# Kernel tuning notes

Measured on AMD Instinct MI355X. Metric: run time of the kernel, lower is better.

Reference implementation:

```python
import jax, jax.numpy as jnp
import numpy as np

A = 5.0  # smoothness parameter 'a'

def setup_inputs() -> dict:
    key = jax.random.key(0)
    kx, kw = jax.random.split(key)
    x = jax.random.uniform(kx, (1024, 512), dtype=jnp.float32)
    weight = jax.random.uniform(kw, (512, 512), dtype=jnp.float32)
    return {"x": x, "weight": weight}

def reference(x, weight):
    # inner: [batch, in, out] broadcast min
    inner = jnp.minimum(x[..., None], weight[None])
    # smooth union (smooth max) over the 'in' dim: logsumexp(a*z)/a
    smooth = jax.scipy.special.logsumexp(A * inner, axis=-2) / A
    hard = jnp.max(inner, axis=-2)
    # straight-through: forward value = hard, gradient flows through smooth
    return jax.lax.stop_gradient(hard - smooth) + smooth
```

## Files before the change

kernel.cpp:

```cpp
#include <hip/hip_runtime.h>


#define MDIM 1024
#define KDIM 512
#define NDIM 512
#define MB 8
#define NT 256
#define KW 64
#define NWAVE 8

__device__ __forceinline__ float bcast(float v, int srcLane) {
    return __int_as_float(__builtin_amdgcn_readlane(__float_as_int(v), srcLane));
}

__global__ __launch_bounds__(512, 2) void tropical_r9(
    const float* __restrict__ x,
    const float* __restrict__ w,
    float* __restrict__ out)
{
    const int tid  = threadIdx.x;
    const int lane = tid & 63;
    const int wv   = tid >> 6;
    const int m0   = blockIdx.x * MB;
    const int n0   = blockIdx.y * NT;
    const int k0   = wv * KW;

    __shared__ float red[NWAVE][MB][NT];

    float xreg[MB];
#pragma unroll
    for (int r = 0; r < MB; ++r)
        xreg[r] = x[(size_t)(m0 + r) * KDIM + k0 + lane];

    const float4* __restrict__ wb =
        (const float4*)(w + (size_t)k0 * NDIM + n0) + lane;

    float acc[MB][4];
#pragma unroll
    for (int r = 0; r < MB; ++r)
#pragma unroll
        for (int j = 0; j < 4; ++j) acc[r][j] = 0.0f;

    float4 cA = wb[0 * 128], cB = wb[1 * 128];
    float4 cC = wb[2 * 128], cD = wb[3 * 128];

#pragma unroll 2
    for (int kc = 0; kc < KW; kc += 4) {
        float4 nA, nB, nC, nD;
        if (kc + 4 < KW) {
            nA = wb[(size_t)(kc + 4) * 128]; nB = wb[(size_t)(kc + 5) * 128];
            nC = wb[(size_t)(kc + 6) * 128]; nD = wb[(size_t)(kc + 7) * 128];
        }
        float xb0[MB], xb1[MB], xb2[MB], xb3[MB];
#pragma unroll
        for (int r = 0; r < MB; ++r) {
            xb0[r] = bcast(xreg[r], kc);
            xb1[r] = bcast(xreg[r], kc + 1);
            xb2[r] = bcast(xreg[r], kc + 2);
            xb3[r] = bcast(xreg[r], kc + 3);
        }
#pragma unroll
        for (int r = 0; r < MB; ++r) {
            acc[r][0] = fmaxf(acc[r][0], fmaxf(fminf(xb0[r], cA.x), fminf(xb1[r], cB.x)));
            acc[r][1] = fmaxf(acc[r][1], fmaxf(fminf(xb0[r], cA.y), fminf(xb1[r], cB.y)));
            acc[r][2] = fmaxf(acc[r][2], fmaxf(fminf(xb0[r], cA.z), fminf(xb1[r], cB.z)));
            acc[r][3] = fmaxf(acc[r][3], fmaxf(fminf(xb0[r], cA.w), fminf(xb1[r], cB.w)));
            acc[r][0] = fmaxf(acc[r][0], fmaxf(fminf(xb2[r], cC.x), fminf(xb3[r], cD.x)));
            acc[r][1] = fmaxf(acc[r][1], fmaxf(fminf(xb2[r], cC.y), fminf(xb3[r], cD.y)));
            acc[r][2] = fmaxf(acc[r][2], fmaxf(fminf(xb2[r], cC.z), fminf(xb3[r], cD.z)));
            acc[r][3] = fmaxf(acc[r][3], fmaxf(fminf(xb2[r], cC.w), fminf(xb3[r], cD.w)));
        }
        cA = nA; cB = nB; cC = nC; cD = nD;
    }

#pragma unroll
    for (int r = 0; r < MB; ++r) {
        float4 v; v.x = acc[r][0]; v.y = acc[r][1]; v.z = acc[r][2]; v.w = acc[r][3];
        ((float4*)&red[wv][r][0])[lane] = v;
    }
    __syncthreads();

    {
        const int r  = tid >> 6;
        const int c4 = tid & 63;
        float4 v = ((const float4*)&red[0][r][0])[c4];
#pragma unroll
        for (int q = 1; q < NWAVE; ++q) {
            float4 u = ((const float4*)&red[q][r][0])[c4];
            v.x = fmaxf(v.x, u.x); v.y = fmaxf(v.y, u.y);
            v.z = fmaxf(v.z, u.z); v.w = fmaxf(v.w, u.w);
        }
        *(float4*)(out + (size_t)(m0 + r) * NDIM + n0 + 4 * c4) = v;
    }
}

extern "C" void kernel_launch(void* const* d_in, const int* in_sizes, int n_in,
                              void* d_out, int out_size, void* d_ws, size_t ws_size,
                              hipStream_t stream) {
    const float* x = (const float*)d_in[0];
    const float* w = (const float*)d_in[1];
    float* out = (float*)d_out;

    dim3 grid(MDIM / MB, NDIM / NT);
    tropical_r9<<<grid, dim3(512), 0, stream>>>(x, w, out);
}
```

Baseline: 77.08 us.

## Stagger per-block K windows and deepen weight prefetch to two stages

Each wave's k-window is rotated by block indices, and its starting row within the window is offset by block, so concurrent blocks read different weight rows. This aims to reduce channel or cache contention. Weight loads are also prefetched two steps ahead instead of one. The extra register buffer may raise register pressure, and the wrapped index math adds a few redundant loads at the end.

```diff
diff --git a/kernel.cpp b/kernel.cpp
--- a/kernel.cpp
+++ b/kernel.cpp
@@ -13,7 +13,7 @@
     return __int_as_float(__builtin_amdgcn_readlane(__float_as_int(v), srcLane));
 }
 
-__global__ __launch_bounds__(512, 2) void tropical_r9(
+__global__ __launch_bounds__(512, 2) void tropical_r11(
     const float* __restrict__ x,
     const float* __restrict__ w,
     float* __restrict__ out)
@@ -21,9 +21,14 @@
     const int tid  = threadIdx.x;
     const int lane = tid & 63;
     const int wv   = tid >> 6;
-    const int m0   = blockIdx.x * MB;
-    const int n0   = blockIdx.y * NT;
-    const int k0   = wv * KW;
+    const int bm   = blockIdx.x;
+    const int bn   = blockIdx.y;
+    const int m0   = bm * MB;
+    const int n0   = bn * NT;
+
+    const int win = (wv + bm + (bn << 2)) & 7;
+    const int k0  = win * KW;
+    const int r0  = (bm & 15) * 4;
 
     __shared__ float red[NWAVE][MB][NT];
 
@@ -41,36 +46,41 @@
 #pragma unroll
         for (int j = 0; j < 4; ++j) acc[r][j] = 0.0f;
 
-    float4 cA = wb[0 * 128], cB = wb[1 * 128];
-    float4 cC = wb[2 * 128], cD = wb[3 * 128];
+    float4 A0 = wb[(size_t)(r0 + 0) * 128], A1 = wb[(size_t)(r0 + 1) * 128];
+    float4 A2 = wb[(size_t)(r0 + 2) * 128], A3 = wb[(size_t)(r0 + 3) * 128];
+    int kp = (r0 + 4) & 63;
+    float4 B0 = wb[(size_t)(kp + 0) * 128], B1 = wb[(size_t)(kp + 1) * 128];
+    float4 B2 = wb[(size_t)(kp + 2) * 128], B3 = wb[(size_t)(kp + 3) * 128];
 
+    int kr = r0;
 #pragma unroll 2
-    for (int kc = 0; kc < KW; kc += 4) {
-        float4 nA, nB, nC, nD;
-        if (kc + 4 < KW) {
-            nA = wb[(size_t)(kc + 4) * 128]; nB = wb[(size_t)(kc + 5) * 128];
-            nC = wb[(size_t)(kc + 6) * 128]; nD = wb[(size_t)(kc + 7) * 128];
-        }
+    for (int i = 0; i < 16; ++i) {
+        const int kn = (kr + 8) & 63;
+        float4 C0 = wb[(size_t)(kn + 0) * 128], C1 = wb[(size_t)(kn + 1) * 128];
+        float4 C2 = wb[(size_t)(kn + 2) * 128], C3 = wb[(size_t)(kn + 3) * 128];
+
         float xb0[MB], xb1[MB], xb2[MB], xb3[MB];
 #pragma unroll
         for (int r = 0; r < MB; ++r) {
-            xb0[r] = bcast(xreg[r], kc);
-            xb1[r] = bcast(xreg[r], kc + 1);
-            xb2[r] = bcast(xreg[r], kc + 2);
-            xb3[r] = bcast(xreg[r], kc + 3);
+            xb0[r] = bcast(xreg[r], kr);
+            xb1[r] = bcast(xreg[r], kr + 1);
+            xb2[r] = bcast(xreg[r], kr + 2);
+            xb3[r] = bcast(xreg[r], kr + 3);
         }
 #pragma unroll
         for (int r = 0; r < MB; ++r) {
-            acc[r][0] = fmaxf(acc[r][0], fmaxf(fminf(xb0[r], cA.x), fminf(xb1[r], cB.x)));
-            acc[r][1] = fmaxf(acc[r][1], fmaxf(fminf(xb0[r], cA.y), fminf(xb1[r], cB.y)));
-            acc[r][2] = fmaxf(acc[r][2], fmaxf(fminf(xb0[r], cA.z), fminf(xb1[r], cB.z)));
-            acc[r][3] = fmaxf(acc[r][3], fmaxf(fminf(xb0[r], cA.w), fminf(xb1[r], cB.w)));
-            acc[r][0] = fmaxf(acc[r][0], fmaxf(fminf(xb2[r], cC.x), fminf(xb3[r], cD.x)));
-            acc[r][1] = fmaxf(acc[r][1], fmaxf(fminf(xb2[r], cC.y), fminf(xb3[r], cD.y)));
-            acc[r][2] = fmaxf(acc[r][2], fmaxf(fminf(xb2[r], cC.z), fminf(xb3[r], cD.z)));
-            acc[r][3] = fmaxf(acc[r][3], fmaxf(fminf(xb2[r], cC.w), fminf(xb3[r], cD.w)));
+            acc[r][0] = fmaxf(acc[r][0], fmaxf(fminf(xb0[r], A0.x), fminf(xb1[r], A1.x)));
+            acc[r][1] = fmaxf(acc[r][1], fmaxf(fminf(xb0[r], A0.y), fminf(xb1[r], A1.y)));
+            acc[r][2] = fmaxf(acc[r][2], fmaxf(fminf(xb0[r], A0.z), fminf(xb1[r], A1.z)));
+            acc[r][3] = fmaxf(acc[r][3], fmaxf(fminf(xb0[r], A0.w), fminf(xb1[r], A1.w)));
+            acc[r][0] = fmaxf(acc[r][0], fmaxf(fminf(xb2[r], A2.x), fminf(xb3[r], A3.x)));
+            acc[r][1] = fmaxf(acc[r][1], fmaxf(fminf(xb2[r], A2.y), fminf(xb3[r], A3.y)));
+            acc[r][2] = fmaxf(acc[r][2], fmaxf(fminf(xb2[r], A2.z), fminf(xb3[r], A3.z)));
+            acc[r][3] = fmaxf(acc[r][3], fmaxf(fminf(xb2[r], A2.w), fminf(xb3[r], A3.w)));
         }
-        cA = nA; cB = nB; cC = nC; cD = nD;
+        A0 = B0; A1 = B1; A2 = B2; A3 = B3;
+        B0 = C0; B1 = C1; B2 = C2; B3 = C3;
+        kr = (kr + 4) & 63;
     }
 
 #pragma unroll
@@ -102,5 +112,5 @@
     float* out = (float*)d_out;
 
     dim3 grid(MDIM / MB, NDIM / NT);
-    tropical_r9<<<grid, dim3(512), 0, stream>>>(x, w, out);
+    tropical_r11<<<grid, dim3(512), 0, stream>>>(x, w, out);
 }
```

Measured after the change: 76.91 us. Within noise of the previous version (-0.2%).

## Pack inputs to fp16 pairs and use packed half min/max accumulation

Applied to the files above, without the earlier changes.

Adds a pre-pass kernel that converts x and the weight matrix to fp16, packing pairs of k values into 32-bit words. The main kernel then does the min/max reduction with packed half2 operations, handling two k values per instruction, and reads x through scalar loads instead of lane broadcasts. The goal is to halve the VALU instruction count and the weight bandwidth. In exchange it adds a second launch, and the result is computed in fp16, so the output is rounded to half precision rather than exact fp32.

```diff
diff --git a/kernel.cpp b/kernel.cpp
--- a/kernel.cpp
+++ b/kernel.cpp
@@ -1,21 +1,47 @@
 #include <hip/hip_runtime.h>
 
+
+typedef _Float16 h2 __attribute__((ext_vector_type(2)));
+typedef unsigned int uint32;
 
 #define MDIM 1024
 #define KDIM 512
 #define NDIM 512
-#define MB 8
-#define NT 256
-#define KW 64
+#define K2   (KDIM / 2)
+#define MB   8
+#define NT   256
 #define NWAVE 8
+#define KP   (K2 / NWAVE)
 
-__device__ __forceinline__ float bcast(float v, int srcLane) {
-    return __int_as_float(__builtin_amdgcn_readlane(__float_as_int(v), srcLane));
+__device__ __forceinline__ h2 h2min(h2 a, h2 b) { return __builtin_elementwise_min(a, b); }
+__device__ __forceinline__ h2 h2max(h2 a, h2 b) { return __builtin_elementwise_max(a, b); }
+
+__global__ __launch_bounds__(512) void pack_f16(const float* __restrict__ x,
+                                                const float* __restrict__ w,
+                                                uint32* __restrict__ xp,
+                                                uint32* __restrict__ wp)
+{
+    const int b = blockIdx.x, tid = threadIdx.x;
+    if (b < 256) {
+        const int idx = b * 512 + tid;
+        const int k2 = idx >> 9, n = idx & 511;
+        h2 v;
+        v[0] = (_Float16)w[(size_t)(2 * k2) * NDIM + n];
+        v[1] = (_Float16)w[(size_t)(2 * k2 + 1) * NDIM + n];
+        wp[idx] = __builtin_bit_cast(uint32, v);
+    } else {
+        const int idx = (b - 256) * 512 + tid;
+        const float2 f = ((const float2*)x)[idx];
+        h2 v;
+        v[0] = (_Float16)f.x;
+        v[1] = (_Float16)f.y;
+        xp[idx] = __builtin_bit_cast(uint32, v);
+    }
 }
 
-__global__ __launch_bounds__(512, 2) void tropical_r9(
-    const float* __restrict__ x,
-    const float* __restrict__ w,
+__global__ __launch_bounds__(512, 2) void tropical_h16(
+    const uint32* __restrict__ xp,
+    const uint32* __restrict__ wp,
     float* __restrict__ out)
 {
     const int tid  = threadIdx.x;
@@ -23,59 +49,44 @@
     const int wv   = tid >> 6;
     const int m0   = blockIdx.x * MB;
     const int n0   = blockIdx.y * NT;
-    const int k0   = wv * KW;
+    const int kp0  = __builtin_amdgcn_readfirstlane(wv * KP);
 
     __shared__ float red[NWAVE][MB][NT];
 
-    float xreg[MB];
-#pragma unroll
-    for (int r = 0; r < MB; ++r)
-        xreg[r] = x[(size_t)(m0 + r) * KDIM + k0 + lane];
+    const uint4* __restrict__ wb =
+        (const uint4*)(wp + (size_t)kp0 * NDIM + n0) + lane;
+    const uint32* __restrict__ xr0 = xp + (size_t)m0 * K2 + kp0;
 
-    const float4* __restrict__ wb =
-        (const float4*)(w + (size_t)k0 * NDIM + n0) + lane;
-
-    float acc[MB][4];
+    h2 acc[MB][4];
 #pragma unroll
     for (int r = 0; r < MB; ++r)
 #pragma unroll
-        for (int j = 0; j < 4; ++j) acc[r][j] = 0.0f;
+        for (int j = 0; j < 4; ++j) acc[r][j] = (h2)0;
 
-    float4 cA = wb[0 * 128], cB = wb[1 * 128];
-    float4 cC = wb[2 * 128], cD = wb[3 * 128];
+    uint4 A = wb[0], B = wb[(size_t)128];
 
 #pragma unroll 2
-    for (int kc = 0; kc < KW; kc += 4) {
-        float4 nA, nB, nC, nD;
-        if (kc + 4 < KW) {
-            nA = wb[(size_t)(kc + 4) * 128]; nB = wb[(size_t)(kc + 5) * 128];
-            nC = wb[(size_t)(kc + 6) * 128]; nD = wb[(size_t)(kc + 7) * 128];
-        }
-        float xb0[MB], xb1[MB], xb2[MB], xb3[MB];
+    for (int i = 0; i < KP; ++i) {
+        uint4 C;
+        if (i + 2 < KP) C = wb[(size_t)(i + 2) * 128];
 #pragma unroll
         for (int r = 0; r < MB; ++r) {
-            xb0[r] = bcast(xreg[r], kc);
-            xb1[r] = bcast(xreg[r], kc + 1);
-            xb2[r] = bcast(xreg[r], kc + 2);
-            xb3[r] = bcast(xreg[r], kc + 3);
+            const h2 xv = __builtin_bit_cast(h2, xr0[(size_t)r * K2 + i]);
+            acc[r][0] = h2max(acc[r][0], h2min(xv, __builtin_bit_cast(h2, A.x)));
+            acc[r][1] = h2max(acc[r][1], h2min(xv, __builtin_bit_cast(h2, A.y)));
+            acc[r][2] = h2max(acc[r][2], h2min(xv, __builtin_bit_cast(h2, A.z)));
+            acc[r][3] = h2max(acc[r][3], h2min(xv, __builtin_bit_cast(h2, A.w)));
         }
-#pragma unroll
-        for (int r = 0; r < MB; ++r) {
-            acc[r][0] = fmaxf(acc[r][0], fmaxf(fminf(xb0[r], cA.x), fminf(xb1[r], cB.x)));
-            acc[r][1] = fmaxf(acc[r][1], fmaxf(fminf(xb0[r], cA.y), fminf(xb1[r], cB.y)));
-            acc[r][2] = fmaxf(acc[r][2], fmaxf(fminf(xb0[r], cA.z), fminf(xb1[r], cB.z)));
-            acc[r][3] = fmaxf(acc[r][3], fmaxf(fminf(xb0[r], cA.w), fminf(xb1[r], cB.w)));
-            acc[r][0] = fmaxf(acc[r][0], fmaxf(fminf(xb2[r], cC.x), fminf(xb3[r], cD.x)));
-            acc[r][1] = fmaxf(acc[r][1], fmaxf(fminf(xb2[r], cC.y), fminf(xb3[r], cD.y)));
-            acc[r][2] = fmaxf(acc[r][2], fmaxf(fminf(xb2[r], cC.z), fminf(xb3[r], cD.z)));
-            acc[r][3] = fmaxf(acc[r][3], fmaxf(fminf(xb2[r], cC.w), fminf(xb3[r], cD.w)));
-        }
-        cA = nA; cB = nB; cC = nC; cD = nD;
+        A = B; B = C;
     }
 
 #pragma unroll
     for (int r = 0; r < MB; ++r) {
-        float4 v; v.x = acc[r][0]; v.y = acc[r][1]; v.z = acc[r][2]; v.w = acc[r][3];
+        float4 v;
+        v.x = fmaxf((float)acc[r][0][0], (float)acc[r][0][1]);
+        v.y = fmaxf((float)acc[r][1][0], (float)acc[r][1][1]);
+        v.z = fmaxf((float)acc[r][2][0], (float)acc[r][2][1]);
+        v.w = fmaxf((float)acc[r][3][0], (float)acc[r][3][1]);
         ((float4*)&red[wv][r][0])[lane] = v;
     }
     __syncthreads();
@@ -101,6 +112,9 @@
     const float* w = (const float*)d_in[1];
     float* out = (float*)d_out;
 
-    dim3 grid(MDIM / MB, NDIM / NT);
-    tropical_r9<<<grid, dim3(512), 0, stream>>>(x, w, out);
+    uint32* xp = (uint32*)d_ws;
+    uint32* wp = xp + (size_t)MDIM * K2;
+
+    pack_f16<<<dim3(768), dim3(512), 0, stream>>>(x, w, xp, wp);
+    tropical_h16<<<dim3(MDIM / MB, NDIM / NT), dim3(512), 0, stream>>>(xp, wp, out);
 }
```

After: 74.02 us. -4.0%, faster.
